# Kernel tuning notes

Measured on AMD Instinct MI355X. Metric: run time of the kernel, lower is better.

Reference implementation:

```python
import jax, jax.numpy as jnp
import numpy as np

NUM_HEADS = 16
D_K = 64
D_V = 64
D_MODEL = 1024


def setup_inputs() -> dict:
    key = jax.random.key(0)
    ks = jax.random.split(key, 11)
    B, S = 2, 2048
    s = 0.02
    return {
        "Q": jax.random.normal(ks[0], (B, S, D_MODEL), jnp.float32),
        "K": jax.random.normal(ks[1], (B, S, D_MODEL), jnp.float32),
        "V": jax.random.normal(ks[2], (B, S, D_MODEL), jnp.float32),
        "WQ": jax.random.normal(ks[3], (D_MODEL, NUM_HEADS * D_K), jnp.float32) * s,
        "bQ": jnp.zeros((NUM_HEADS * D_K,), jnp.float32),
        "WK": jax.random.normal(ks[4], (D_MODEL, NUM_HEADS * D_K), jnp.float32) * s,
        "bK": jnp.zeros((NUM_HEADS * D_K,), jnp.float32),
        "WV": jax.random.normal(ks[5], (D_MODEL, NUM_HEADS * D_V), jnp.float32) * s,
        "bV": jnp.zeros((NUM_HEADS * D_V,), jnp.float32),
        "WO": jax.random.normal(ks[6], (NUM_HEADS * D_V, D_MODEL), jnp.float32) * s,
        "bO": jnp.zeros((D_MODEL,), jnp.float32),
    }


def reference(Q, K, V, WQ, bQ, WK, bK, WV, bV, WO, bO):
    B = Q.shape[0]
    # linear projections, then split heads: [B, H, S, d]
    q = (Q @ WQ + bQ).reshape(B, -1, NUM_HEADS, D_K).transpose(0, 2, 1, 3)
    k = (K @ WK + bK).reshape(B, -1, NUM_HEADS, D_K).transpose(0, 2, 1, 3)
    v = (V @ WV + bV).reshape(B, -1, NUM_HEADS, D_V).transpose(0, 2, 1, 3)
    # unfused attention: full [B, H, Sq, Sk] score matrix
    scores = jnp.einsum("bhqd,bhkd->bhqk", q, k) / jnp.sqrt(jnp.float32(D_K))
    attn = jax.nn.softmax(scores, axis=-1)  # dropout is identity in eval mode
    out = jnp.einsum("bhqk,bhkd->bhqd", attn, v)
    out = out.transpose(0, 2, 1, 3).reshape(B, -1, NUM_HEADS * D_V)
    return out @ WO + bO
```

## Files before the change

kernel.cpp:

```cpp
#include <hip/hip_runtime.h>
#include <hip/hip_bf16.h>
#include <stdint.h>

#define BATCH 2
#define SEQ   2048
#define NH    16
#define DH    64
#define DM    1024
#define MR    (BATCH * SEQ)

typedef __bf16 bf16_t;
typedef bf16_t bf16x4 __attribute__((ext_vector_type(4)));
typedef bf16_t bf16x8 __attribute__((ext_vector_type(8)));
typedef float  f32x4  __attribute__((ext_vector_type(4)));
typedef float  f32x16 __attribute__((ext_vector_type(16)));

typedef const __attribute__((address_space(1))) void* gas_t;
typedef       __attribute__((address_space(3))) void* las_t;

__device__ __forceinline__ void gload16(const void* g, void* l) {
  __builtin_amdgcn_global_load_lds((gas_t)g, (las_t)l, 16, 0, 0);
}

__device__ __forceinline__ float fast_exp2(float x) {
#if __has_builtin(__builtin_amdgcn_exp2f)
  return __builtin_amdgcn_exp2f(x);
#else
  float r; asm volatile("v_exp_f32 %0, %1\n\ts_nop 1" : "=v"(r) : "v"(x)); return r;
#endif
}

#define GL(dst, base, OFF) \
  asm volatile("global_load_dwordx4 %0, %1, off offset:" #OFF : "=v"(dst) : "v"(base))
#define WAITV(N) asm volatile("s_waitcnt vmcnt(" #N ")" ::: "memory")
#define SCHED0 __builtin_amdgcn_sched_barrier(0)

__global__ __launch_bounds__(256) void cvt3_kernel(const float* __restrict__ x0,
                                                   const float* __restrict__ x1,
                                                   const float* __restrict__ x2,
                                                   bf16_t* __restrict__ y0,
                                                   bf16_t* __restrict__ y1,
                                                   bf16_t* __restrict__ y2, int n) {
  const int z = blockIdx.y;
  const float* x = z == 0 ? x0 : (z == 1 ? x1 : x2);
  bf16_t*      y = z == 0 ? y0 : (z == 1 ? y1 : y2);
  int i = (blockIdx.x * 256 + threadIdx.x) * 8;
  if (i + 8 <= n) {
    float4 a = *(const float4*)(x + i);
    float4 b = *(const float4*)(x + i + 4);
    bf16x8 o;
    o[0] = (bf16_t)a.x; o[1] = (bf16_t)a.y; o[2] = (bf16_t)a.z; o[3] = (bf16_t)a.w;
    o[4] = (bf16_t)b.x; o[5] = (bf16_t)b.y; o[6] = (bf16_t)b.z; o[7] = (bf16_t)b.w;
    *(bf16x8*)(y + i) = o;
  }
}

__global__ __launch_bounds__(256) void wtrans4_kernel(const float* __restrict__ W0,
                                                      const float* __restrict__ W1,
                                                      const float* __restrict__ W2,
                                                      const float* __restrict__ W3,
                                                      bf16_t* __restrict__ T0,
                                                      bf16_t* __restrict__ T1,
                                                      bf16_t* __restrict__ T2,
                                                      bf16_t* __restrict__ T3) {
  const int z = blockIdx.z;
  const float* W = z == 0 ? W0 : (z == 1 ? W1 : (z == 2 ? W2 : W3));
  bf16_t*     Wt = z == 0 ? T0 : (z == 1 ? T1 : (z == 2 ? T2 : T3));
  __shared__ bf16_t t[64][65];
  const int c0 = blockIdx.x * 64, r0 = blockIdx.y * 64;
  const int tid = threadIdx.x;
  const int r = tid >> 2, cc = (tid & 3) * 16;
  const float* src = W + (size_t)(r0 + r) * DM + c0 + cc;
#pragma unroll
  for (int i = 0; i < 16; ++i) t[r][cc + i] = (bf16_t)src[i];
  __syncthreads();
  bf16_t* dst = Wt + (size_t)(c0 + r) * DM + r0 + cc;
#pragma unroll
  for (int i = 0; i < 16; ++i) dst[i] = t[cc + i][r];
}

__global__ __launch_bounds__(256) void gemm3_kernel(
    const bf16_t* __restrict__ A0, const bf16_t* __restrict__ A1,
    const bf16_t* __restrict__ A2,
    const bf16_t* __restrict__ B0, const bf16_t* __restrict__ B1,
    const bf16_t* __restrict__ B2,
    const float* __restrict__ bi0, const float* __restrict__ bi1,
    const float* __restrict__ bi2,
    float s0, float s1, float s2,
    bf16_t* __restrict__ C0, bf16_t* __restrict__ C1, bf16_t* __restrict__ C2) {
  const int z = blockIdx.z;
  const bf16_t* A    = z == 0 ? A0 : (z == 1 ? A1 : A2);
  const bf16_t* Bt   = z == 0 ? B0 : (z == 1 ? B1 : B2);
  const float*  bias = z == 0 ? bi0 : (z == 1 ? bi1 : bi2);
  const float   scale = z == 0 ? s0 : (z == 1 ? s1 : s2);
  bf16_t*       C    = z == 0 ? C0 : (z == 1 ? C1 : C2);
  const int K = DM, N = DM;

  __shared__ __attribute__((aligned(16))) bf16_t As[128 * 64];
  __shared__ __attribute__((aligned(16))) bf16_t Bs[128 * 64];
  const int m0 = blockIdx.x * 128, n0 = blockIdx.y * 128;
  const int tid = threadIdx.x;
  const int wave = tid >> 6, lane = tid & 63;
  const int lm = lane & 15, lg = lane >> 4;
  const int wr = wave >> 1, wc = wave & 1;
  f32x4 acc[4][4];
#pragma unroll
  for (int a = 0; a < 4; ++a)
#pragma unroll
    for (int bb = 0; bb < 4; ++bb) acc[a][bb] = (f32x4){0.f, 0.f, 0.f, 0.f};

  for (int k0 = 0; k0 < K; k0 += 64) {
    __syncthreads();
#pragma unroll
    for (int i = 0; i < 4; ++i) {
      const int c = tid + i * 256;
      const int row = c >> 3, j = c & 7, js = j ^ (row & 7);
      gload16(A  + (size_t)(m0 + row) * K + k0 + js * 8,
              As + (size_t)(wave * 64 + i * 256) * 8);
      gload16(Bt + (size_t)(n0 + row) * K + k0 + js * 8,
              Bs + (size_t)(wave * 64 + i * 256) * 8);
    }
    asm volatile("s_waitcnt vmcnt(0)" ::: "memory");
    __syncthreads();
#pragma unroll
    for (int kk = 0; kk < 2; ++kk) {
      bf16x8 af[4], bfr[4];
#pragma unroll
      for (int t = 0; t < 4; ++t) {
        const int ra = wr * 64 + t * 16 + lm;
        af[t] = *(const bf16x8*)((const char*)As + ra * 128 +
                                 ((kk * 64 + lg * 16) ^ ((ra & 7) << 4)));
        const int rb = wc * 64 + t * 16 + lm;
        bfr[t] = *(const bf16x8*)((const char*)Bs + rb * 128 +
                                  ((kk * 64 + lg * 16) ^ ((rb & 7) << 4)));
      }
      __builtin_amdgcn_s_setprio(1);
#pragma unroll
      for (int mf = 0; mf < 4; ++mf)
#pragma unroll
        for (int nf = 0; nf < 4; ++nf)
          acc[mf][nf] = __builtin_amdgcn_mfma_f32_16x16x32_bf16(af[mf], bfr[nf],
                                                                acc[mf][nf], 0, 0, 0);
      __builtin_amdgcn_s_setprio(0);
    }
  }
#pragma unroll
  for (int mf = 0; mf < 4; ++mf)
#pragma unroll
    for (int nf = 0; nf < 4; ++nf) {
      const int col = n0 + wc * 64 + nf * 16 + lm;
      const float bv = bias[col];
#pragma unroll
      for (int i = 0; i < 4; ++i) {
        const int row = m0 + wr * 64 + mf * 16 + lg * 4 + i;
        const float val = (acc[mf][nf][i] + bv) * scale;
        size_t off;
        if (z == 0) {
          off = (size_t)row * N + col;
        } else {
          const int bb = row >> 11, s = row & (SEQ - 1);
          const int hh = col >> 6, d = col & 63;
          const size_t base = (size_t)(bb * NH + hh) * (SEQ * DH);
          if (z == 1) {
            off = base + ((((size_t)(s >> 6) * 2 + ((s >> 5) & 1)) * 4 + (d >> 4)) * 64
                          + ((d >> 3) & 1) * 32 + (s & 31)) * 8 + (d & 7);
          } else {
            off = base + ((((size_t)(s >> 6) * 2 + (d >> 5)) * 4 + ((s >> 4) & 3)) * 64
                          + ((s >> 3) & 1) * 32 + (d & 31)) * 8 + (s & 7);
          }
        }
        C[off] = (bf16_t)val;
      }
    }
}

template <int OUT_BF16>
__global__ __launch_bounds__(256) void gemm_kernel(const bf16_t* __restrict__ A,
                                                   const bf16_t* __restrict__ Bt,
                                                   const float* __restrict__ bias,
                                                   float scale,
                                                   void* __restrict__ Cv,
                                                   int K, int N) {
  __shared__ __attribute__((aligned(16))) bf16_t As[64 * 64];
  __shared__ __attribute__((aligned(16))) bf16_t Bs[128 * 64];
  const int m0 = blockIdx.x * 64, n0 = blockIdx.y * 128;
  const int tid = threadIdx.x;
  const int wave = tid >> 6, lane = tid & 63;
  const int lm = lane & 15, lg = lane >> 4;
  const int wr = wave >> 1, wc = wave & 1;
  f32x4 acc[2][4];
#pragma unroll
  for (int a = 0; a < 2; ++a)
#pragma unroll
    for (int bb = 0; bb < 4; ++bb) acc[a][bb] = (f32x4){0.f, 0.f, 0.f, 0.f};

  for (int k0 = 0; k0 < K; k0 += 64) {
    __syncthreads();
#pragma unroll
    for (int i = 0; i < 2; ++i) {
      const int c = tid + i * 256;
      const int row = c >> 3, j = c & 7, js = j ^ (row & 7);
      gload16(A + (size_t)(m0 + row) * K + k0 + js * 8,
              As + (size_t)(wave * 64 + i * 256) * 8);
    }
#pragma unroll
    for (int i = 0; i < 4; ++i) {
      const int c = tid + i * 256;
      const int row = c >> 3, j = c & 7, js = j ^ (row & 7);
      gload16(Bt + (size_t)(n0 + row) * K + k0 + js * 8,
              Bs + (size_t)(wave * 64 + i * 256) * 8);
    }
    asm volatile("s_waitcnt vmcnt(0)" ::: "memory");
    __syncthreads();
#pragma unroll
    for (int kk = 0; kk < 2; ++kk) {
      bf16x8 af[2], bfr[4];
#pragma unroll
      for (int t = 0; t < 2; ++t) {
        const int ra = wr * 32 + t * 16 + lm;
        af[t] = *(const bf16x8*)((const char*)As + ra * 128 +
                                 ((kk * 64 + lg * 16) ^ ((ra & 7) << 4)));
      }
#pragma unroll
      for (int t = 0; t < 4; ++t) {
        const int rb = wc * 64 + t * 16 + lm;
        bfr[t] = *(const bf16x8*)((const char*)Bs + rb * 128 +
                                  ((kk * 64 + lg * 16) ^ ((rb & 7) << 4)));
      }
      __builtin_amdgcn_s_setprio(1);
#pragma unroll
      for (int mf = 0; mf < 2; ++mf)
#pragma unroll
        for (int nf = 0; nf < 4; ++nf)
          acc[mf][nf] = __builtin_amdgcn_mfma_f32_16x16x32_bf16(af[mf], bfr[nf],
                                                                acc[mf][nf], 0, 0, 0);
      __builtin_amdgcn_s_setprio(0);
    }
  }
#pragma unroll
  for (int mf = 0; mf < 2; ++mf)
#pragma unroll
    for (int nf = 0; nf < 4; ++nf) {
      const int col = n0 + wc * 64 + nf * 16 + lm;
      const float bv = bias[col];
#pragma unroll
      for (int i = 0; i < 4; ++i) {
        const int row = m0 + wr * 32 + mf * 16 + lg * 4 + i;
        const float val = (acc[mf][nf][i] + bv) * scale;
        if (OUT_BF16) ((bf16_t*)Cv)[(size_t)row * N + col] = (bf16_t)val;
        else          ((float*)Cv)[(size_t)row * N + col] = val;
      }
    }
}

__device__ __forceinline__ void issue8(bf16x8 (&f)[8], const bf16_t* p) {
  const bf16_t* p2 = p + 2048;
  GL(f[0], p, 0); GL(f[1], p, 1024); GL(f[2], p, 2048); GL(f[3], p, 3072);
  GL(f[4], p2, 0); GL(f[5], p2, 1024); GL(f[6], p2, 2048); GL(f[7], p2, 3072);
}

__device__ __forceinline__ void qk_only(const bf16x8 (&kf)[8], const bf16x8 (&qf)[4],
                                        f32x16 (&sc)[2]) {
#pragma unroll
  for (int r = 0; r < 16; ++r) { sc[0][r] = 0.f; sc[1][r] = 0.f; }
  __builtin_amdgcn_s_setprio(1);
#pragma unroll
  for (int ds = 0; ds < 4; ++ds) {
    sc[0] = __builtin_amdgcn_mfma_f32_32x32x16_bf16(kf[ds],     qf[ds], sc[0], 0, 0, 0);
    sc[1] = __builtin_amdgcn_mfma_f32_32x32x16_bf16(kf[4 + ds], qf[ds], sc[1], 0, 0, 0);
  }
  __builtin_amdgcn_s_setprio(0);
}

__device__ __forceinline__ void softmax_store(f32x16 (&sc)[2], float& lrun,
                                              char* __restrict__ PsW,
                                              int lq, int hi) {
#pragma unroll
  for (int kt = 0; kt < 2; ++kt)
#pragma unroll
    for (int r = 0; r < 16; ++r) sc[kt][r] = fast_exp2(sc[kt][r]);
#pragma unroll
  for (int kt = 0; kt < 2; ++kt)
#pragma unroll
    for (int g = 0; g < 4; ++g) {
      bf16x4 pw;
      pw[0] = (bf16_t)sc[kt][4 * g + 0]; pw[1] = (bf16_t)sc[kt][4 * g + 1];
      pw[2] = (bf16_t)sc[kt][4 * g + 2]; pw[3] = (bf16_t)sc[kt][4 * g + 3];
      *(bf16x4*)(PsW + lq * 128 +
                 ((kt * 64 + g * 16 + hi * 8) ^ ((lq & 7) << 4))) = pw;
    }
  float s8[8];
#pragma unroll
  for (int r = 0; r < 8; ++r)
    s8[r] = (sc[0][r] + sc[0][r + 8]) + (sc[1][r] + sc[1][r + 8]);
  float s = ((s8[0] + s8[4]) + (s8[1] + s8[5])) +
            ((s8[2] + s8[6]) + (s8[3] + s8[7]));
  s += __shfl_xor(s, 32);
  lrun += s;
}

__device__ __forceinline__ void pv_step(const bf16x8 (&vf)[8], f32x16 (&acc)[2],
                                        char* __restrict__ PsW, int lq, int hi) {
#pragma unroll
  for (int ks = 0; ks < 4; ++ks) {
    bf16x8 pf = *(const bf16x8*)(PsW + lq * 128 +
                                 ((ks * 32 + hi * 16) ^ ((lq & 7) << 4)));
    __builtin_amdgcn_s_setprio(1);
    acc[0] = __builtin_amdgcn_mfma_f32_32x32x16_bf16(pf, vf[ks],     acc[0], 0, 0, 0);
    acc[1] = __builtin_amdgcn_mfma_f32_32x32x16_bf16(pf, vf[4 + ks], acc[1], 0, 0, 0);
    __builtin_amdgcn_s_setprio(0);
  }
}

__global__ __launch_bounds__(256, 2) void flash_kernel(const bf16_t* __restrict__ q,
                                                       const bf16_t* __restrict__ kF,
                                                       const bf16_t* __restrict__ vF,
                                                       bf16_t* __restrict__ o) {
  __shared__ __attribute__((aligned(16))) bf16_t Ps[4][32 * 64];
  const int wg = blockIdx.x;
  const int swz = (wg & 7) * 64 + (wg >> 3);
  const int qt = swz & 15, h = (swz >> 4) & 15, b = swz >> 8;
  const int tid = threadIdx.x;
  const int wave = tid >> 6, lane = tid & 63;
  const int lq = lane & 31, hi = lane >> 5;
  char* PsW = (char*)(&Ps[wave][0]);

  const bf16_t* qb = q + (size_t)(b * SEQ + qt * 128 + wave * 32) * DM + h * DH;
  const bf16_t* kb = kF + (size_t)(b * NH + h) * (SEQ * DH) + lane * 8;
  const bf16_t* vb = vF + (size_t)(b * NH + h) * (SEQ * DH) + lane * 8;

  bf16x8 qf[4];
#pragma unroll
  for (int ds = 0; ds < 4; ++ds)
    qf[ds] = *(const bf16x8*)(qb + (size_t)lq * DM + ds * 16 + hi * 8);

  f32x16 acc[2];
#pragma unroll
  for (int r = 0; r < 16; ++r) { acc[0][r] = 0.f; acc[1][r] = 0.f; }
  float lrun = 0.f;

  bf16x8 kA[8], kB[8], vv[8];
  f32x16 scC[2], scN[2];

  issue8(kA, kb);
  WAITV(0); SCHED0;
  issue8(kB, kb + 4096);
  issue8(vv, vb);
  qk_only(kA, qf, scC);

  const int NT = SEQ / 64;
  for (int t = 0; t < NT; t += 2) {
    WAITV(8); SCHED0;
    qk_only(kB, qf, scN);
    softmax_store(scC, lrun, PsW, lq, hi);
    WAITV(0); SCHED0;
    pv_step(vv, acc, PsW, lq, hi);
    {
      const int tn = (t + 2 < NT) ? t + 2 : NT - 1;
      issue8(kA, kb + (size_t)tn * 4096);
    }
    issue8(vv, vb + (size_t)(t + 1) * 4096);
    WAITV(8); SCHED0;
    qk_only(kA, qf, scC);
    softmax_store(scN, lrun, PsW, lq, hi);
    WAITV(0); SCHED0;
    pv_step(vv, acc, PsW, lq, hi);
    {
      const int tn = (t + 3 < NT) ? t + 3 : NT - 1;
      issue8(kB, kb + (size_t)tn * 4096);
    }
    if (t + 2 < NT) issue8(vv, vb + (size_t)(t + 2) * 4096);
  }
  asm volatile("s_waitcnt vmcnt(0)" ::: "memory");

  const float inv = __builtin_amdgcn_rcpf(lrun);
#pragma unroll
  for (int r = 0; r < 16; ++r) {
    const int qrow = (r & 3) + 8 * (r >> 2) + 4 * hi;
    const float iv = __shfl(inv, qrow);
    const int row = b * SEQ + qt * 128 + wave * 32 + qrow;
#pragma unroll
    for (int dt = 0; dt < 2; ++dt) {
      const int col = h * DH + dt * 32 + lq;
      o[(size_t)row * DM + col] = (bf16_t)(acc[dt][r] * iv);
    }
  }
}

extern "C" void kernel_launch(void* const* d_in, const int* in_sizes, int n_in,
                              void* d_out, int out_size, void* d_ws, size_t ws_size,
                              hipStream_t stream) {
  (void)in_sizes; (void)n_in; (void)out_size; (void)ws_size;
  const float* Q  = (const float*)d_in[0];
  const float* Kx = (const float*)d_in[1];
  const float* V  = (const float*)d_in[2];
  const float* WQ = (const float*)d_in[3];
  const float* bQ = (const float*)d_in[4];
  const float* WK = (const float*)d_in[5];
  const float* bK = (const float*)d_in[6];
  const float* WV = (const float*)d_in[7];
  const float* bV = (const float*)d_in[8];
  const float* WO = (const float*)d_in[9];
  const float* bO = (const float*)d_in[10];

  const size_t MS  = (size_t)MR * DM;
  const size_t WSZ = (size_t)DM * DM;
  bf16_t* ws  = (bf16_t*)d_ws;
  bf16_t* Qb  = ws;
  bf16_t* Kb  = Qb + MS;
  bf16_t* Vb  = Kb + MS;
  bf16_t* WQt = Vb + MS;
  bf16_t* WKt = WQt + WSZ;
  bf16_t* WVt = WKt + WSZ;
  bf16_t* WOt = WVt + WSZ;
  bf16_t* qp  = WOt + WSZ;
  bf16_t* kp  = qp + MS;
  bf16_t* vp  = kp + MS;
  bf16_t* ao  = Kb;

  const float scale_q = 0.125f * 1.44269504088896340736f;

  cvt3_kernel<<<dim3((unsigned)(MS / 2048), 3), 256, 0, stream>>>(Q, Kx, V, Qb, Kb, Vb, (int)MS);
  wtrans4_kernel<<<dim3(16, 16, 4), 256, 0, stream>>>(WQ, WK, WV, WO, WQt, WKt, WVt, WOt);

  gemm3_kernel<<<dim3(32, 8, 3), 256, 0, stream>>>(Qb, Kb, Vb,
                                                   WQt, WKt, WVt,
                                                   bQ, bK, bV,
                                                   scale_q, 1.0f, 1.0f,
                                                   qp, kp, vp);

  flash_kernel<<<dim3(512), 256, 0, stream>>>(qp, kp, vp, ao);
  gemm_kernel<0><<<dim3(MR / 64, DM / 128), 256, 0, stream>>>(ao, WOt, bO, 1.0f, d_out, DM, DM);
}
```

Measured before the change: 126.6 us.

## Split flash attention KV range in two and add a combine kernel

The flash kernel now runs twice as many workgroups, each covering half of the key/value sequence. Each writes its unnormalized accumulator in bf16 and its row sum to workspace. A new combine kernel adds the two partials, normalizes, and writes the head-interleaved output for the output projection. The aim is more parallelism and better load balance, at the cost of an extra launch, extra partial-result memory traffic and a doubled pipeline prologue per tile.

```diff
diff --git a/kernel.cpp b/kernel.cpp
--- a/kernel.cpp
+++ b/kernel.cpp
@@ -8,6 +8,7 @@
 #define DH    64
 #define DM    1024
 #define MR    (BATCH * SEQ)
+#define BHS   65536
 
 typedef __bf16 bf16_t;
 typedef bf16_t bf16x4 __attribute__((ext_vector_type(4)));
@@ -315,11 +316,13 @@
 __global__ __launch_bounds__(256, 2) void flash_kernel(const bf16_t* __restrict__ q,
                                                        const bf16_t* __restrict__ kF,
                                                        const bf16_t* __restrict__ vF,
-                                                       bf16_t* __restrict__ o) {
+                                                       bf16_t* __restrict__ pacc,
+                                                       float* __restrict__ pl) {
   __shared__ __attribute__((aligned(16))) bf16_t Ps[4][32 * 64];
   const int wg = blockIdx.x;
-  const int swz = (wg & 7) * 64 + (wg >> 3);
-  const int qt = swz & 15, h = (swz >> 4) & 15, b = swz >> 8;
+  const int flat = (wg & 7) * 128 + (wg >> 3);
+  const int qt = flat & 15, h = (flat >> 4) & 15;
+  const int b = (flat >> 8) & 1, split = flat >> 9;
   const int tid = threadIdx.x;
   const int wave = tid >> 6, lane = tid & 63;
   const int lq = lane & 31, hi = lane >> 5;
@@ -342,21 +345,22 @@
   bf16x8 kA[8], kB[8], vv[8];
   f32x16 scC[2], scN[2];
 
-  issue8(kA, kb);
+  const int t0 = split * 16, tend = t0 + 16;
+
+  issue8(kA, kb + (size_t)t0 * 4096);
   WAITV(0); SCHED0;
-  issue8(kB, kb + 4096);
-  issue8(vv, vb);
+  issue8(kB, kb + (size_t)(t0 + 1) * 4096);
+  issue8(vv, vb + (size_t)t0 * 4096);
   qk_only(kA, qf, scC);
 
-  const int NT = SEQ / 64;
-  for (int t = 0; t < NT; t += 2) {
+  for (int t = t0; t < tend; t += 2) {
     WAITV(8); SCHED0;
     qk_only(kB, qf, scN);
     softmax_store(scC, lrun, PsW, lq, hi);
     WAITV(0); SCHED0;
     pv_step(vv, acc, PsW, lq, hi);
     {
-      const int tn = (t + 2 < NT) ? t + 2 : NT - 1;
+      const int tn = (t + 2 < tend) ? t + 2 : tend - 1;
       issue8(kA, kb + (size_t)tn * 4096);
     }
     issue8(vv, vb + (size_t)(t + 1) * 4096);
@@ -366,25 +370,39 @@
     WAITV(0); SCHED0;
     pv_step(vv, acc, PsW, lq, hi);
     {
-      const int tn = (t + 3 < NT) ? t + 3 : NT - 1;
+      const int tn = (t + 3 < tend) ? t + 3 : tend - 1;
       issue8(kB, kb + (size_t)tn * 4096);
     }
-    if (t + 2 < NT) issue8(vv, vb + (size_t)(t + 2) * 4096);
+    if (t + 2 < tend) issue8(vv, vb + (size_t)(t + 2) * 4096);
   }
   asm volatile("s_waitcnt vmcnt(0)" ::: "memory");
 
-  const float inv = __builtin_amdgcn_rcpf(lrun);
+  const size_t bhqbase = (size_t)(b * NH + h) * SEQ + qt * 128 + wave * 32;
+  bf16_t* pa = pacc + ((size_t)split * BHS + bhqbase) * 64;
 #pragma unroll
   for (int r = 0; r < 16; ++r) {
     const int qrow = (r & 3) + 8 * (r >> 2) + 4 * hi;
-    const float iv = __shfl(inv, qrow);
-    const int row = b * SEQ + qt * 128 + wave * 32 + qrow;
-#pragma unroll
-    for (int dt = 0; dt < 2; ++dt) {
-      const int col = h * DH + dt * 32 + lq;
-      o[(size_t)row * DM + col] = (bf16_t)(acc[dt][r] * iv);
-    }
-  }
+#pragma unroll
+    for (int dt = 0; dt < 2; ++dt)
+      pa[(size_t)qrow * 64 + dt * 32 + lq] = (bf16_t)acc[dt][r];
+  }
+  if (hi == 0) pl[(size_t)split * BHS + bhqbase + lq] = lrun;
+}
+
+__global__ __launch_bounds__(256) void combine_kernel(const bf16_t* __restrict__ pacc,
+                                                      const float* __restrict__ pl,
+                                                      bf16_t* __restrict__ ao) {
+  const int tid = blockIdx.x * 256 + threadIdx.x;
+  const int bhq = tid >> 3, d0 = (tid & 7) * 8;
+  const float inv = __builtin_amdgcn_rcpf(pl[bhq] + pl[BHS + bhq]);
+  bf16x8 x0 = *(const bf16x8*)(pacc + (size_t)bhq * 64 + d0);
+  bf16x8 x1 = *(const bf16x8*)(pacc + (size_t)BHS * 64 + (size_t)bhq * 64 + d0);
+  const int qq = bhq & (SEQ - 1), hh = (bhq >> 11) & (NH - 1), bb = bhq >> 15;
+  bf16x8 o8;
+#pragma unroll
+  for (int j = 0; j < 8; ++j)
+    o8[j] = (bf16_t)(((float)x0[j] + (float)x1[j]) * inv);
+  *(bf16x8*)(ao + (size_t)(bb * SEQ + qq) * DM + hh * DH + d0) = o8;
 }
 
 extern "C" void kernel_launch(void* const* d_in, const int* in_sizes, int n_in,
@@ -416,7 +434,9 @@
   bf16_t* qp  = WOt + WSZ;
   bf16_t* kp  = qp + MS;
   bf16_t* vp  = kp + MS;
-  bf16_t* ao  = Kb;
+  bf16_t* pacc = Qb;
+  bf16_t* ao  = Vb;
+  float*  pl  = (float*)WQt;
 
   const float scale_q = 0.125f * 1.44269504088896340736f;
 
@@ -429,6 +449,7 @@
                                                    scale_q, 1.0f, 1.0f,
                                                    qp, kp, vp);
 
-  flash_kernel<<<dim3(512), 256, 0, stream>>>(qp, kp, vp, ao);
+  flash_kernel<<<dim3(1024), 256, 0, stream>>>(qp, kp, vp, pacc, pl);
+  combine_kernel<<<dim3(2048), 256, 0, stream>>>(pacc, pl, ao);
   gemm_kernel<0><<<dim3(MR / 64, DM / 128), 256, 0, stream>>>(ao, WOt, bO, 1.0f, d_out, DM, DM);
 }
```

After: 134.2 us. 1.06x slower.
